# Optimization experiments

Hardware: AMD Instinct MI355X
Metric: run time of the kernel (lower is better)

Reference implementation:

```python
import jax, jax.numpy as jnp
import numpy as np

LN_EPS = 1e-5

def _ln(x, g, b):
    m = x.mean(-1, keepdims=True)
    v = ((x - m) ** 2).mean(-1, keepdims=True)
    return (x - m) * jax.lax.rsqrt(v + LN_EPS) * g + b

def setup_inputs() -> dict:
    key = jax.random.key(0)
    B, Q, K, H, NH, L = 4, 32, 8192, 1024, 16, 128
    ks = jax.random.split(key, 10)
    def p(k, shape):
        return jax.random.normal(k, shape, jnp.float32) * 0.02
    return {
        "question_emb": jax.random.normal(ks[0], (B, Q, H), jnp.float32),
        "context_emb": jax.random.normal(ks[1], (B, K, H), jnp.float32),
        "Wq_l": p(ks[2], (H, H)), "bq_l": jnp.zeros((H,), jnp.float32),
        "Wk_l": p(ks[3], (H, H)), "bk_l": jnp.zeros((H,), jnp.float32),
        "Wq_g": p(ks[4], (H, H)), "bq_g": jnp.zeros((H,), jnp.float32),
        "Wk_g": p(ks[5], (H, H)), "bk_g": jnp.zeros((H,), jnp.float32),
        "ln_g": jnp.ones((H,), jnp.float32), "ln_b": jnp.zeros((H,), jnp.float32),
        "gp_W1": p(ks[6], (2 * H, H)), "gp_b1": jnp.zeros((H,), jnp.float32),
        "gp_W2": p(ks[7], (H, 1)), "gp_b2": jnp.zeros((1,), jnp.float32),
        "num_heads": NH,
        "chunk_len": L,
    }

def reference(question_emb, context_emb, Wq_l, bq_l, Wk_l, bk_l,
              Wq_g, bq_g, Wk_g, bk_g, ln_g, ln_b,
              gp_W1, gp_b1, gp_W2, gp_b2, num_heads, chunk_len):
    B, Qn, H = question_emb.shape
    K = context_emb.shape[1]
    nh, L = num_heads, chunk_len
    d = H // nh
    J = K // L
    scale = 1.0 / np.sqrt(d)

    # ---- Global scorer: one cross-attn over all K, then per-chunk mean pooling ----
    qh = (question_emb @ Wq_g + bq_g).reshape(B, Qn, nh, d).transpose(0, 2, 1, 3)   # [B,nh,Q,d]
    kh = (context_emb @ Wk_g + bk_g).reshape(B, K, nh, d).transpose(0, 2, 1, 3)     # [B,nh,K,d]
    wg = jax.nn.softmax(jnp.einsum('bhqd,bhkd->bhqk', qh, kh) * scale, axis=-1)     # [B,nh,Q,K]
    attn = wg.mean(axis=(1, 2))                                                     # [B,K]
    global_scores = jax.nn.softmax(attn.reshape(B, J, L).mean(-1), axis=-1)         # [B,J]

    # ---- Local scorer: per-chunk cross-attn (batched over chunks), max-over-keys pooling ----
    qh_l = (question_emb @ Wq_l + bq_l).reshape(B, Qn, nh, d).transpose(0, 2, 1, 3)  # [B,nh,Q,d]
    kh_l = (context_emb @ Wk_l + bk_l).reshape(B, J, L, nh, d).transpose(0, 1, 3, 2, 4)  # [B,J,nh,L,d]
    s_l = jnp.einsum('bhqd,bjhld->bjhql', qh_l, kh_l) * scale                        # [B,J,nh,Q,L]
    w_l = jax.nn.softmax(s_l, axis=-1)
    local_scores = jax.nn.softmax(w_l.max(-1).mean(axis=(2, 3)), axis=-1)            # [B,J]

    # ---- Router: LN'd mean-pool vecs -> gate MLP -> fuse -> softmax ----
    q_vec = _ln(question_emb.mean(1), ln_g, ln_b)                                    # [B,H]
    c_vec = _ln(context_emb.reshape(B, J, L, H).mean(2), ln_g, ln_b)                 # [B,J,H]
    g_in = jnp.concatenate([jnp.broadcast_to(q_vec[:, None, :], (B, J, H)), c_vec], -1)
    h1 = jax.nn.gelu(g_in @ gp_W1 + gp_b1, approximate=False)
    gate = jax.nn.sigmoid(h1 @ gp_W2 + gp_b2)[..., 0]                                # [B,J]
    fused = gate * local_scores + (1.0 - gate) * global_scores
    final_scores = jax.nn.softmax(fused, axis=-1)                                    # [B,J]
    global_gate = final_scores.mean(-1).reshape(B, 1, 1)
    return final_scores, local_scores, global_scores, global_gate
```

## Files before the change

kernel.cpp:

```cpp
#include <hip/hip_runtime.h>
#include <math.h>

#define B_    4
#define QN    32
#define KN    8192
#define HDIM  1024
#define NHD   16
#define DH    64
#define LCH   128
#define JCH   64

typedef float f32x4 __attribute__((ext_vector_type(4)));
typedef short s16x8 __attribute__((ext_vector_type(8)));
typedef unsigned short u16;

__device__ __forceinline__ u16 f2bf(float f) {
  unsigned u = __float_as_uint(f);
  u += 0x7fffu + ((u >> 16) & 1u);
  return (u16)(u >> 16);
}

__device__ __forceinline__ float bf2f(u16 v) {
  return __uint_as_float(((unsigned)v) << 16);
}

__device__ __forceinline__ void llds16(const void* g, void* l) {
  __builtin_amdgcn_global_load_lds((const __attribute__((address_space(1))) unsigned int*)g,
                                   (__attribute__((address_space(3))) unsigned int*)l,
                                   16, 0, 0);
}

__global__ __launch_bounds__(256) void k_zero(float* __restrict__ qh, float* __restrict__ h1,
                                              float* __restrict__ qpart) {
  int i = blockIdx.x * 256 + threadIdx.x;
  float4 z = make_float4(0.f, 0.f, 0.f, 0.f);
  if (i < 65536)        ((float4*)qh)[i] = z;
  else if (i < 131072)  ((float4*)h1)[i - 65536] = z;
  else if (i < 132096)  ((float4*)qpart)[i - 131072] = z;
}

__global__ __launch_bounds__(256) void k_ctxcv(const float* __restrict__ ctx, u16* __restrict__ ctxb,
                                               const float* __restrict__ g, const float* __restrict__ lb,
                                               float* __restrict__ cvec) {
  int bj = blockIdx.x, t = threadIdx.x;
  const float* p = ctx + (size_t)bj * LCH * HDIM + t * 4;
  u16* op = ctxb + (size_t)bj * LCH * HDIM + t * 4;
  float a0 = 0, a1 = 0, a2 = 0, a3 = 0;
  for (int r = 0; r < LCH; ++r) {
    float4 v = *(const float4*)(p + (size_t)r * HDIM);
    ushort4 o;
    o.x = f2bf(v.x); o.y = f2bf(v.y); o.z = f2bf(v.z); o.w = f2bf(v.w);
    *(ushort4*)(op + (size_t)r * HDIM) = o;
    a0 += v.x; a1 += v.y; a2 += v.z; a3 += v.w;
  }
  const float sc = 1.0f / LCH;
  a0 *= sc; a1 *= sc; a2 *= sc; a3 *= sc;
  float s = a0 + a1 + a2 + a3;
  float ss = a0 * a0 + a1 * a1 + a2 * a2 + a3 * a3;
#pragma unroll
  for (int o = 1; o < 64; o <<= 1) { s += __shfl_xor(s, o, 64); ss += __shfl_xor(ss, o, 64); }
  __shared__ float sm[4], sq[4];
  int wid = t >> 6, lane = t & 63;
  if (lane == 0) { sm[wid] = s; sq[wid] = ss; }
  __syncthreads();
  float S = sm[0] + sm[1] + sm[2] + sm[3], SS = sq[0] + sq[1] + sq[2] + sq[3];
  float mu = S / HDIM;
  float inv = rsqrtf(SS / HDIM - mu * mu + 1e-5f);
  int c = t * 4;
  float4 o;
  o.x = (a0 - mu) * inv * g[c + 0] + lb[c + 0];
  o.y = (a1 - mu) * inv * g[c + 1] + lb[c + 1];
  o.z = (a2 - mu) * inv * g[c + 2] + lb[c + 2];
  o.w = (a3 - mu) * inv * g[c + 3] + lb[c + 3];
  *(float4*)&cvec[(size_t)bj * HDIM + c] = o;
}

__global__ __launch_bounds__(256) void k_gemm_f32(const float* __restrict__ A, int lda,
                                                  const float* __restrict__ Bm, int ldb,
                                                  float* __restrict__ C, int ldc, int kchunk) {
  __shared__ float As[64][17];
  __shared__ float Bs[16][64];
  int t = threadIdx.x;
  int m0 = blockIdx.x * 64, n0 = blockIdx.y * 64, k0 = blockIdx.z * kchunk;
  int tm = t >> 4, tn = t & 15;
  float c[4][4];
#pragma unroll
  for (int i = 0; i < 4; ++i)
#pragma unroll
    for (int j = 0; j < 4; ++j) c[i][j] = 0.f;
  int ra = t >> 2, ka = (t & 3) * 4;
  int kb = t >> 4, nb = (t & 15) * 4;
  for (int kk = 0; kk < kchunk; kk += 16) {
    float4 va = *(const float4*)(A + (size_t)(m0 + ra) * lda + k0 + kk + ka);
    float4 vb = *(const float4*)(Bm + (size_t)(k0 + kk + kb) * ldb + n0 + nb);
    As[ra][ka] = va.x; As[ra][ka + 1] = va.y; As[ra][ka + 2] = va.z; As[ra][ka + 3] = va.w;
    *(float4*)&Bs[kb][nb] = vb;
    __syncthreads();
#pragma unroll
    for (int kq = 0; kq < 16; ++kq) {
      float a0 = As[tm * 4 + 0][kq], a1 = As[tm * 4 + 1][kq];
      float a2 = As[tm * 4 + 2][kq], a3 = As[tm * 4 + 3][kq];
      float b0 = Bs[kq][tn * 4 + 0], b1 = Bs[kq][tn * 4 + 1];
      float b2 = Bs[kq][tn * 4 + 2], b3 = Bs[kq][tn * 4 + 3];
      c[0][0] += a0 * b0; c[0][1] += a0 * b1; c[0][2] += a0 * b2; c[0][3] += a0 * b3;
      c[1][0] += a1 * b0; c[1][1] += a1 * b1; c[1][2] += a1 * b2; c[1][3] += a1 * b3;
      c[2][0] += a2 * b0; c[2][1] += a2 * b1; c[2][2] += a2 * b2; c[2][3] += a2 * b3;
      c[3][0] += a3 * b0; c[3][1] += a3 * b1; c[3][2] += a3 * b2; c[3][3] += a3 * b3;
    }
    __syncthreads();
  }
#pragma unroll
  for (int i = 0; i < 4; ++i)
#pragma unroll
    for (int j = 0; j < 4; ++j)
      atomicAdd(&C[(size_t)(m0 + tm * 4 + i) * ldc + n0 + tn * 4 + j], c[i][j]);
}

__global__ __launch_bounds__(256) void k_gemm_qh(const float* __restrict__ A,
                                                 const float* __restrict__ Bg, const float* __restrict__ Bl,
                                                 float* __restrict__ C) {
  __shared__ float As[64][17];
  __shared__ float Bs[16][64];
  int t = threadIdx.x;
  int ny = blockIdx.y;
  const float* Bm = (ny < 16) ? Bg : Bl;
  float* Cp = (ny < 16) ? C : (C + 131072);
  int m0 = blockIdx.x * 64, n0 = (ny & 15) * 64, k0 = blockIdx.z * 128;
  int tm = t >> 4, tn = t & 15;
  float c[4][4];
#pragma unroll
  for (int i = 0; i < 4; ++i)
#pragma unroll
    for (int j = 0; j < 4; ++j) c[i][j] = 0.f;
  int ra = t >> 2, ka = (t & 3) * 4;
  int kb = t >> 4, nb = (t & 15) * 4;
  for (int kk = 0; kk < 128; kk += 16) {
    float4 va = *(const float4*)(A + (size_t)(m0 + ra) * HDIM + k0 + kk + ka);
    float4 vb = *(const float4*)(Bm + (size_t)(k0 + kk + kb) * HDIM + n0 + nb);
    As[ra][ka] = va.x; As[ra][ka + 1] = va.y; As[ra][ka + 2] = va.z; As[ra][ka + 3] = va.w;
    *(float4*)&Bs[kb][nb] = vb;
    __syncthreads();
#pragma unroll
    for (int kq = 0; kq < 16; ++kq) {
      float a0 = As[tm * 4 + 0][kq], a1 = As[tm * 4 + 1][kq];
      float a2 = As[tm * 4 + 2][kq], a3 = As[tm * 4 + 3][kq];
      float b0 = Bs[kq][tn * 4 + 0], b1 = Bs[kq][tn * 4 + 1];
      float b2 = Bs[kq][tn * 4 + 2], b3 = Bs[kq][tn * 4 + 3];
      c[0][0] += a0 * b0; c[0][1] += a0 * b1; c[0][2] += a0 * b2; c[0][3] += a0 * b3;
      c[1][0] += a1 * b0; c[1][1] += a1 * b1; c[1][2] += a1 * b2; c[1][3] += a1 * b3;
      c[2][0] += a2 * b0; c[2][1] += a2 * b1; c[2][2] += a2 * b2; c[2][3] += a2 * b3;
      c[3][0] += a3 * b0; c[3][1] += a3 * b1; c[3][2] += a3 * b2; c[3][3] += a3 * b3;
    }
    __syncthreads();
  }
#pragma unroll
  for (int i = 0; i < 4; ++i)
#pragma unroll
    for (int j = 0; j < 4; ++j)
      atomicAdd(&Cp[(size_t)(m0 + tm * 4 + i) * HDIM + n0 + tn * 4 + j], c[i][j]);
}

__global__ __launch_bounds__(256) void k_afold(const float* __restrict__ qh, const float* __restrict__ Wk_g,
                                               const float* __restrict__ Wk_l, const float* __restrict__ bq_g,
                                               const float* __restrict__ bq_l, u16* __restrict__ Ab) {
  int ct = blockIdx.x;
  int slot = blockIdx.y;
  int b = blockIdx.z;
  int s2 = slot >> 4, h = slot & 15;
  const float* qhp = qh + (size_t)(s2 * 4 + b) * QN * HDIM;
  const float* Wk = s2 ? Wk_l : Wk_g;
  const float* bq = s2 ? bq_l : bq_g;
  __shared__ float qs[QN][DH];
  int t = threadIdx.x;
  {
    int q = t >> 3, doff = (t & 7) * 8;
    const float4* src = (const float4*)(qhp + (size_t)q * HDIM + h * DH + doff);
    float4 b0 = *(const float4*)(bq + h * DH + doff);
    float4 b1 = *(const float4*)(bq + h * DH + doff + 4);
    float4 v0 = src[0], v1 = src[1];
    qs[q][doff + 0] = v0.x + b0.x; qs[q][doff + 1] = v0.y + b0.y;
    qs[q][doff + 2] = v0.z + b0.z; qs[q][doff + 3] = v0.w + b0.w;
    qs[q][doff + 4] = v1.x + b1.x; qs[q][doff + 5] = v1.y + b1.y;
    qs[q][doff + 6] = v1.z + b1.z; qs[q][doff + 7] = v1.w + b1.w;
  }
  __syncthreads();
  int c = ct * 256 + t;
  float w[DH];
  const float* wr = Wk + (size_t)c * HDIM + h * DH;
#pragma unroll
  for (int d = 0; d < DH; d += 4) {
    float4 v = *(const float4*)(wr + d);
    w[d] = v.x; w[d + 1] = v.y; w[d + 2] = v.z; w[d + 3] = v.w;
  }
  u16* outp = Ab + ((size_t)b * HDIM + s2 * 512 + h * QN) * HDIM + c;
  for (int q = 0; q < QN; ++q) {
    float acc = 0.f;
#pragma unroll
    for (int d = 0; d < DH; ++d) acc += qs[q][d] * w[d];
    outp[(size_t)q * HDIM] = f2bf(acc * 0.125f);
  }
}

__global__ __launch_bounds__(256) void k_sbias(const float* __restrict__ qh, const float* __restrict__ bk_g,
                                               const float* __restrict__ bk_l, const float* __restrict__ bq_g,
                                               const float* __restrict__ bq_l, float* __restrict__ sbias) {
  int i = blockIdx.x * 256 + threadIdx.x;
  int b = i >> 10, n = i & (HDIM - 1);
  int s2 = n >> 9, hq = n & 511, h = hq >> 5, q = hq & 31;
  const float* qr = qh + ((size_t)(s2 * 4 + b) * QN + q) * HDIM + h * DH;
  const float* bk = (s2 ? bk_l : bk_g) + h * DH;
  const float* bq = (s2 ? bq_l : bq_g) + h * DH;
  float acc = 0.f;
#pragma unroll
  for (int d = 0; d < DH; ++d) acc += (qr[d] + bq[d]) * bk[d];
  sbias[i] = acc * 0.125f;
}

__global__ __launch_bounds__(512, 2) void k_scores(const u16* __restrict__ ctxb, const u16* __restrict__ Ab,
                                                   const float* __restrict__ sbias,
                                                   float* __restrict__ mglob, float* __restrict__ zglob,
                                                   float* __restrict__ locinv) {
  __shared__ u16 lds[65536];
  u16* A0 = lds;           u16* B0 = lds + 16384;
  u16* A1 = lds + 32768;   u16* B1 = lds + 49152;
  int bid = blockIdx.x;
  int work = (bid & 7) * 64 + (bid >> 3);
  int b = work >> 7, rem = work & 127, rt = rem >> 2, nt = rem & 3;
  int t = threadIdx.x, wid = t >> 6, lane = t & 63;
  int wm = wid >> 2, wn = wid & 3;
  int lrow = lane & 15, lkg = lane >> 4;

  const u16* ctx0 = ctxb + ((size_t)b * KN + rt * 256) * HDIM;
  const u16* Afp  = Ab + ((size_t)b * HDIM + nt * 256) * HDIM;

  int grow = wid * 8 + (lane >> 3);
  int gslot = (lane & 7) ^ (lane >> 3);
  const u16* gA[4]; const u16* gB[4]; int dof[4];
#pragma unroll
  for (int s = 0; s < 4; ++s) {
    gA[s] = ctx0 + (size_t)(s * 64 + grow) * HDIM + gslot * 8;
    gB[s] = Afp + (size_t)(s * 64 + grow) * HDIM + gslot * 8;
    dof[s] = s * 4096 + wid * 512;
  }

  int rowA = (wm * 128 + lrow) * 64;
  int rowB = (wn * 64 + lrow) * 64;
  int p8[2];
#pragma unroll
  for (int ks = 0; ks < 2; ++ks) p8[ks] = ((ks * 4 + lkg) ^ (lane & 7)) * 8;

  f32x4 acc[8][4];
#pragma unroll
  for (int mi = 0; mi < 8; ++mi)
#pragma unroll
    for (int ni = 0; ni < 4; ++ni) acc[mi][ni] = 0.f;

#define STAGE(AT, BT, KT) { \
  _Pragma("unroll") for (int s = 0; s < 4; ++s) { \
    llds16(gA[s] + (KT) * 64, (AT) + dof[s]); \
    llds16(gB[s] + (KT) * 64, (BT) + dof[s]); } }

#define COMPUTE(AT, BT) { \
  _Pragma("unroll") for (int ks = 0; ks < 2; ++ks) { \
    const u16* pA = (AT) + rowA + p8[ks]; \
    const u16* pB = (BT) + rowB + p8[ks]; \
    s16x8 av[8], bv[4]; \
    _Pragma("unroll") for (int mi = 0; mi < 8; ++mi) av[mi] = *(const s16x8*)(pA + mi * 1024); \
    _Pragma("unroll") for (int ni = 0; ni < 4; ++ni) bv[ni] = *(const s16x8*)(pB + ni * 1024); \
    _Pragma("unroll") for (int mi = 0; mi < 8; ++mi) \
    _Pragma("unroll") for (int ni = 0; ni < 4; ++ni) \
      acc[mi][ni] = __builtin_amdgcn_mfma_f32_16x16x32_bf16(av[mi], bv[ni], acc[mi][ni], 0, 0, 0); } }

#define SYNCN(N) { asm volatile("s_waitcnt vmcnt(" #N ")" ::: "memory"); \
                   __builtin_amdgcn_s_barrier(); \
                   __builtin_amdgcn_sched_barrier(0); }

#define SUB(KT, CA, CB, SA, SB, FULL) { \
  if (FULL) { STAGE(SA, SB, (KT) + 1); } \
  if (FULL) { SYNCN(8) } else { SYNCN(0) } \
  __builtin_amdgcn_s_setprio(1); \
  COMPUTE(CA, CB); \
  __builtin_amdgcn_s_setprio(0); \
  __builtin_amdgcn_s_barrier(); }

  STAGE(A0, B0, 0);
  SUB(0,  A0, B0, A1, B1, 1)
  SUB(1,  A1, B1, A0, B0, 1)
  SUB(2,  A0, B0, A1, B1, 1)
  SUB(3,  A1, B1, A0, B0, 1)
  SUB(4,  A0, B0, A1, B1, 1)
  SUB(5,  A1, B1, A0, B0, 1)
  SUB(6,  A0, B0, A1, B1, 1)
  SUB(7,  A1, B1, A0, B0, 1)
  SUB(8,  A0, B0, A1, B1, 1)
  SUB(9,  A1, B1, A0, B0, 1)
  SUB(10, A0, B0, A1, B1, 1)
  SUB(11, A1, B1, A0, B0, 1)
  SUB(12, A0, B0, A1, B1, 1)
  SUB(13, A1, B1, A0, B0, 1)
  SUB(14, A0, B0, A1, B1, 1)
  SUB(15, A1, B1, A0, B0, 0)
#undef STAGE
#undef COMPUTE
#undef SYNCN
#undef SUB

  int jc = rt * 2 + wm;
  float sb[4];
#pragma unroll
  for (int ni = 0; ni < 4; ++ni)
    sb[ni] = sbias[b * HDIM + nt * 256 + wn * 64 + ni * 16 + lrow];
#pragma unroll
  for (int ni = 0; ni < 4; ++ni) {
    float m = -1e30f;
#pragma unroll
    for (int mi = 0; mi < 8; ++mi)
#pragma unroll
      for (int r = 0; r < 4; ++r) m = fmaxf(m, acc[mi][ni][r]);
    m += sb[ni];
    m = fmaxf(m, __shfl_xor(m, 16, 64));
    m = fmaxf(m, __shfl_xor(m, 32, 64));
    float z = 0.f;
#pragma unroll
    for (int mi = 0; mi < 8; ++mi)
#pragma unroll
      for (int r = 0; r < 4; ++r) z += __expf(acc[mi][ni][r] + sb[ni] - m);
    z += __shfl_xor(z, 16, 64);
    z += __shfl_xor(z, 32, 64);
    if (lane < 16) {
      int n = nt * 256 + wn * 64 + ni * 16 + lane;
      if (n < 512) {
        size_t o = ((size_t)b * 512 + n) * JCH + jc;
        mglob[o] = m; zglob[o] = z;
      } else {
        locinv[((size_t)b * JCH + jc) * 512 + (n - 512)] = 1.0f / z;
      }
    }
  }
}

__global__ __launch_bounds__(256) void k_qvec(const float* __restrict__ q, const float* __restrict__ g,
                                              const float* __restrict__ lb, float* __restrict__ qvec) {
  int b = blockIdx.x, t = threadIdx.x;
  const float* p = q + (size_t)b * QN * HDIM + t * 4;
  float a0 = 0, a1 = 0, a2 = 0, a3 = 0;
  for (int r = 0; r < QN; ++r) {
    float4 v = *(const float4*)(p + (size_t)r * HDIM);
    a0 += v.x; a1 += v.y; a2 += v.z; a3 += v.w;
  }
  const float sc = 1.0f / QN;
  a0 *= sc; a1 *= sc; a2 *= sc; a3 *= sc;
  float s = a0 + a1 + a2 + a3;
  float ss = a0 * a0 + a1 * a1 + a2 * a2 + a3 * a3;
#pragma unroll
  for (int o = 1; o < 64; o <<= 1) { s += __shfl_xor(s, o, 64); ss += __shfl_xor(ss, o, 64); }
  __shared__ float sm[4], sq[4];
  int wid = t >> 6, lane = t & 63;
  if (lane == 0) { sm[wid] = s; sq[wid] = ss; }
  __syncthreads();
  float S = sm[0] + sm[1] + sm[2] + sm[3], SS = sq[0] + sq[1] + sq[2] + sq[3];
  float mu = S / HDIM;
  float inv = rsqrtf(SS / HDIM - mu * mu + 1e-5f);
  int c = t * 4;
  float4 o;
  o.x = (a0 - mu) * inv * g[c + 0] + lb[c + 0];
  o.y = (a1 - mu) * inv * g[c + 1] + lb[c + 1];
  o.z = (a2 - mu) * inv * g[c + 2] + lb[c + 2];
  o.w = (a3 - mu) * inv * g[c + 3] + lb[c + 3];
  *(float4*)&qvec[(size_t)b * HDIM + c] = o;
}

__global__ __launch_bounds__(256) void k_qpart(const float* __restrict__ qvec, const float* __restrict__ W1,
                                               float* __restrict__ qpart) {
  int nt = blockIdx.x, b = blockIdx.y, ks = blockIdx.z;
  int n = nt * 256 + threadIdx.x;
  const float* qv = qvec + (size_t)b * HDIM + ks * 64;
  const float* wp = W1 + (size_t)ks * 64 * HDIM + n;
  float acc = 0.f;
#pragma unroll 8
  for (int c = 0; c < 64; ++c) acc += qv[c] * wp[(size_t)c * HDIM];
  atomicAdd(&qpart[(size_t)b * HDIM + n], acc);
}

__global__ __launch_bounds__(64) void k_hq(const float* __restrict__ mglob, const float* __restrict__ zglob,
                                           float* __restrict__ Mh, float* __restrict__ Zr) {
  int id = blockIdx.x * 64 + threadIdx.x;
  int b = id >> 9, hq = id & 511;
  const float* mg = mglob + ((size_t)b * 512 + hq) * JCH;
  const float* zg = zglob + ((size_t)b * 512 + hq) * JCH;
  float m = -1e30f;
  for (int j = 0; j < JCH; ++j) m = fmaxf(m, mg[j]);
  float z = 0.f;
  for (int j = 0; j < JCH; ++j) z += zg[j] * __expf(mg[j] - m);
  Mh[id] = m;
  Zr[id] = 1.0f / z;
}

__global__ __launch_bounds__(256) void k_chunk(const float* __restrict__ mglob, const float* __restrict__ zglob,
                                               const float* __restrict__ locinv,
                                               const float* __restrict__ Mh, const float* __restrict__ Zr,
                                               const float* __restrict__ h1, const float* __restrict__ qpart,
                                               const float* __restrict__ b1, const float* __restrict__ W2,
                                               float* __restrict__ abuf, float* __restrict__ lbuf,
                                               float* __restrict__ gbuf) {
  int bj = blockIdx.x, t = threadIdx.x;
  int b = bj >> 6, j = bj & 63;
  const float* mg = mglob + (size_t)b * 512 * JCH + j;
  const float* zg = zglob + (size_t)b * 512 * JCH + j;
  const float* lp = locinv + (size_t)bj * 512;
  const float* Mb = Mh + (size_t)b * 512;
  const float* Zb = Zr + (size_t)b * 512;
  float a = 0.f, l = 0.f, gsum = 0.f;
  for (int hq = t; hq < 512; hq += 256) {
    a += zg[(size_t)hq * JCH] * __expf(mg[(size_t)hq * JCH] - Mb[hq]) * Zb[hq];
    l += lp[hq];
  }
  const float* hp = h1 + (size_t)bj * HDIM;
  const float* qp = qpart + (size_t)b * HDIM;
  for (int n = t; n < HDIM; n += 256) {
    float x = hp[n] + qp[n] + b1[n];
    x = x * 0.5f * (1.0f + erff(x * 0.70710678118654752f));
    gsum += x * W2[n];
  }
#pragma unroll
  for (int o = 1; o < 64; o <<= 1) {
    a += __shfl_xor(a, o, 64); l += __shfl_xor(l, o, 64); gsum += __shfl_xor(gsum, o, 64);
  }
  __shared__ float ra[4], rl[4], rg[4];
  int wid = t >> 6, lane = t & 63;
  if (lane == 0) { ra[wid] = a; rl[wid] = l; rg[wid] = gsum; }
  __syncthreads();
  if (t == 0) {
    abuf[bj] = (ra[0] + ra[1] + ra[2] + ra[3]) * (1.0f / 65536.0f);
    lbuf[bj] = (rl[0] + rl[1] + rl[2] + rl[3]) * (1.0f / 512.0f);
    gbuf[bj] = rg[0] + rg[1] + rg[2] + rg[3];
  }
}

__global__ __launch_bounds__(64) void k_final(const float* __restrict__ abuf, const float* __restrict__ lbuf,
                                              const float* __restrict__ gbuf, const float* __restrict__ b2,
                                              float* __restrict__ out) {
  int b = blockIdx.x, t = threadIdx.x;
  float a = abuf[b * 64 + t];
  float l = lbuf[b * 64 + t];
  float gt = gbuf[b * 64 + t] + b2[0];
  gt = 1.0f / (1.0f + __expf(-gt));
  float am = a, lm = l;
#pragma unroll
  for (int o = 1; o < 64; o <<= 1) { am = fmaxf(am, __shfl_xor(am, o, 64)); lm = fmaxf(lm, __shfl_xor(lm, o, 64)); }
  float ae = __expf(a - am), le = __expf(l - lm);
  float as_ = ae, ls_ = le;
#pragma unroll
  for (int o = 1; o < 64; o <<= 1) { as_ += __shfl_xor(as_, o, 64); ls_ += __shfl_xor(ls_, o, 64); }
  float gs = ae / as_, ls = le / ls_;
  float fu = gt * ls + (1.0f - gt) * gs;
  float fm = fu;
#pragma unroll
  for (int o = 1; o < 64; o <<= 1) fm = fmaxf(fm, __shfl_xor(fm, o, 64));
  float fe = __expf(fu - fm);
  float fs_ = fe;
#pragma unroll
  for (int o = 1; o < 64; o <<= 1) fs_ += __shfl_xor(fs_, o, 64);
  float fv = fe / fs_;
  out[b * 64 + t] = fv;
  out[256 + b * 64 + t] = ls;
  out[512 + b * 64 + t] = gs;
  float tot = fv;
#pragma unroll
  for (int o = 1; o < 64; o <<= 1) tot += __shfl_xor(tot, o, 64);
  if (t == 0) out[768 + b] = tot * (1.0f / 64.0f);
}

extern "C" void kernel_launch(void* const* d_in, const int* in_sizes, int n_in,
                              void* d_out, int out_size, void* d_ws, size_t ws_size,
                              hipStream_t stream) {
  const float* question = (const float*)d_in[0];
  const float* context  = (const float*)d_in[1];
  const float* Wq_l = (const float*)d_in[2];
  const float* bq_l = (const float*)d_in[3];
  const float* Wk_l = (const float*)d_in[4];
  const float* bk_l = (const float*)d_in[5];
  const float* Wq_g = (const float*)d_in[6];
  const float* bq_g = (const float*)d_in[7];
  const float* Wk_g = (const float*)d_in[8];
  const float* bk_g = (const float*)d_in[9];
  const float* ln_g = (const float*)d_in[10];
  const float* ln_b = (const float*)d_in[11];
  const float* W1   = (const float*)d_in[12];
  const float* b1   = (const float*)d_in[13];
  const float* W2   = (const float*)d_in[14];
  const float* b2   = (const float*)d_in[15];

  char* ws = (char*)d_ws;
  u16*   ctxb   = (u16*)(ws + 0);
  u16*   Ab     = (u16*)(ws + 67108864);
  float* qh     = (float*)(ws + 75497472);
  float* sbias  = (float*)(ws + 76546048);
  float* mglob  = (float*)(ws + 76562432);
  float* zglob  = (float*)(ws + 77086720);
  float* locinv = (float*)(ws + 77611008);
  float* qvec   = (float*)(ws + 78135296);
  float* cvec   = (float*)(ws + 78151680);
  float* qpart  = (float*)(ws + 79200256);
  float* h1     = (float*)(ws + 79216640);
  float* Mh     = (float*)(ws + 80265216);
  float* Zr     = (float*)(ws + 80273408);
  float* abuf   = (float*)(ws + 80281600);
  float* lbuf   = (float*)(ws + 80282624);
  float* gbuf   = (float*)(ws + 80283648);

  hipLaunchKernelGGL(k_zero, dim3(516), dim3(256), 0, stream, qh, h1, qpart);
  hipLaunchKernelGGL(k_ctxcv, dim3(256), dim3(256), 0, stream, context, ctxb, ln_g, ln_b, cvec);
  hipLaunchKernelGGL(k_gemm_qh, dim3(2, 32, 8), dim3(256), 0, stream, question, Wq_g, Wq_l, qh);
  hipLaunchKernelGGL(k_afold, dim3(4, 32, 4), dim3(256), 0, stream, qh, Wk_g, Wk_l, bq_g, bq_l, Ab);
  hipLaunchKernelGGL(k_sbias, dim3(16), dim3(256), 0, stream, qh, bk_g, bk_l, bq_g, bq_l, sbias);
  hipLaunchKernelGGL(k_scores, dim3(512), dim3(512), 0, stream, ctxb, Ab, sbias, mglob, zglob, locinv);
  hipLaunchKernelGGL(k_qvec, dim3(4), dim3(256), 0, stream, question, ln_g, ln_b, qvec);
  hipLaunchKernelGGL(k_qpart, dim3(4, 4, 16), dim3(256), 0, stream, qvec, W1, qpart);
  hipLaunchKernelGGL(k_gemm_f32, dim3(4, 16, 8), dim3(256), 0, stream, cvec, HDIM, W1 + 1048576, HDIM, h1, HDIM, 128);
  hipLaunchKernelGGL(k_hq, dim3(32), dim3(64), 0, stream, mglob, zglob, Mh, Zr);
  hipLaunchKernelGGL(k_chunk, dim3(256), dim3(256), 0, stream, mglob, zglob, locinv, Mh, Zr, h1, qpart, b1, W2, abuf, lbuf, gbuf);
  hipLaunchKernelGGL(k_final, dim3(4), dim3(64), 0, stream, abuf, lbuf, gbuf, b2, (float*)d_out);
}
```

Measured before the change: 232.2 us.

## Merge preprocessing kernels into two heterogeneous phase launches and drop split-K atomics

```diff
diff --git a/kernel.cpp b/kernel.cpp
--- a/kernel.cpp
+++ b/kernel.cpp
@@ -20,79 +20,28 @@
   return (u16)(u >> 16);
 }
 
-__device__ __forceinline__ float bf2f(u16 v) {
-  return __uint_as_float(((unsigned)v) << 16);
-}
-
 __device__ __forceinline__ void llds16(const void* g, void* l) {
   __builtin_amdgcn_global_load_lds((const __attribute__((address_space(1))) unsigned int*)g,
                                    (__attribute__((address_space(3))) unsigned int*)l,
                                    16, 0, 0);
 }
 
-__global__ __launch_bounds__(256) void k_zero(float* __restrict__ qh, float* __restrict__ h1,
-                                              float* __restrict__ qpart) {
-  int i = blockIdx.x * 256 + threadIdx.x;
-  float4 z = make_float4(0.f, 0.f, 0.f, 0.f);
-  if (i < 65536)        ((float4*)qh)[i] = z;
-  else if (i < 131072)  ((float4*)h1)[i - 65536] = z;
-  else if (i < 132096)  ((float4*)qpart)[i - 131072] = z;
-}
-
-__global__ __launch_bounds__(256) void k_ctxcv(const float* __restrict__ ctx, u16* __restrict__ ctxb,
-                                               const float* __restrict__ g, const float* __restrict__ lb,
-                                               float* __restrict__ cvec) {
-  int bj = blockIdx.x, t = threadIdx.x;
-  const float* p = ctx + (size_t)bj * LCH * HDIM + t * 4;
-  u16* op = ctxb + (size_t)bj * LCH * HDIM + t * 4;
-  float a0 = 0, a1 = 0, a2 = 0, a3 = 0;
-  for (int r = 0; r < LCH; ++r) {
-    float4 v = *(const float4*)(p + (size_t)r * HDIM);
-    ushort4 o;
-    o.x = f2bf(v.x); o.y = f2bf(v.y); o.z = f2bf(v.z); o.w = f2bf(v.w);
-    *(ushort4*)(op + (size_t)r * HDIM) = o;
-    a0 += v.x; a1 += v.y; a2 += v.z; a3 += v.w;
-  }
-  const float sc = 1.0f / LCH;
-  a0 *= sc; a1 *= sc; a2 *= sc; a3 *= sc;
-  float s = a0 + a1 + a2 + a3;
-  float ss = a0 * a0 + a1 * a1 + a2 * a2 + a3 * a3;
-#pragma unroll
-  for (int o = 1; o < 64; o <<= 1) { s += __shfl_xor(s, o, 64); ss += __shfl_xor(ss, o, 64); }
-  __shared__ float sm[4], sq[4];
-  int wid = t >> 6, lane = t & 63;
-  if (lane == 0) { sm[wid] = s; sq[wid] = ss; }
-  __syncthreads();
-  float S = sm[0] + sm[1] + sm[2] + sm[3], SS = sq[0] + sq[1] + sq[2] + sq[3];
-  float mu = S / HDIM;
-  float inv = rsqrtf(SS / HDIM - mu * mu + 1e-5f);
-  int c = t * 4;
-  float4 o;
-  o.x = (a0 - mu) * inv * g[c + 0] + lb[c + 0];
-  o.y = (a1 - mu) * inv * g[c + 1] + lb[c + 1];
-  o.z = (a2 - mu) * inv * g[c + 2] + lb[c + 2];
-  o.w = (a3 - mu) * inv * g[c + 3] + lb[c + 3];
-  *(float4*)&cvec[(size_t)bj * HDIM + c] = o;
-}
-
-__global__ __launch_bounds__(256) void k_gemm_f32(const float* __restrict__ A, int lda,
-                                                  const float* __restrict__ Bm, int ldb,
-                                                  float* __restrict__ C, int ldc, int kchunk) {
-  __shared__ float As[64][17];
-  __shared__ float Bs[16][64];
+__device__ __forceinline__ void gemm64_direct(const float* __restrict__ A, const float* __restrict__ Bm,
+                                              float* __restrict__ C, int m0, int n0, char* smem) {
+  float (*As)[17] = (float(*)[17])smem;
+  float (*Bs)[64] = (float(*)[64])(smem + 4352);
   int t = threadIdx.x;
-  int m0 = blockIdx.x * 64, n0 = blockIdx.y * 64, k0 = blockIdx.z * kchunk;
   int tm = t >> 4, tn = t & 15;
-  float c[4][4];
-#pragma unroll
-  for (int i = 0; i < 4; ++i)
-#pragma unroll
-    for (int j = 0; j < 4; ++j) c[i][j] = 0.f;
   int ra = t >> 2, ka = (t & 3) * 4;
   int kb = t >> 4, nb = (t & 15) * 4;
-  for (int kk = 0; kk < kchunk; kk += 16) {
-    float4 va = *(const float4*)(A + (size_t)(m0 + ra) * lda + k0 + kk + ka);
-    float4 vb = *(const float4*)(Bm + (size_t)(k0 + kk + kb) * ldb + n0 + nb);
+  float c[4][4];
+#pragma unroll
+  for (int i = 0; i < 4; ++i)
+#pragma unroll
+    for (int j = 0; j < 4; ++j) c[i][j] = 0.f;
+  for (int kk = 0; kk < HDIM; kk += 16) {
+    float4 va = *(const float4*)(A + (size_t)(m0 + ra) * HDIM + kk + ka);
+    float4 vb = *(const float4*)(Bm + (size_t)(kk + kb) * HDIM + n0 + nb);
     As[ra][ka] = va.x; As[ra][ka + 1] = va.y; As[ra][ka + 2] = va.z; As[ra][ka + 3] = va.w;
     *(float4*)&Bs[kb][nb] = vb;
     __syncthreads();
@@ -113,107 +62,160 @@
   for (int i = 0; i < 4; ++i)
 #pragma unroll
     for (int j = 0; j < 4; ++j)
-      atomicAdd(&C[(size_t)(m0 + tm * 4 + i) * ldc + n0 + tn * 4 + j], c[i][j]);
-}
-
-__global__ __launch_bounds__(256) void k_gemm_qh(const float* __restrict__ A,
-                                                 const float* __restrict__ Bg, const float* __restrict__ Bl,
-                                                 float* __restrict__ C) {
-  __shared__ float As[64][17];
-  __shared__ float Bs[16][64];
-  int t = threadIdx.x;
-  int ny = blockIdx.y;
-  const float* Bm = (ny < 16) ? Bg : Bl;
-  float* Cp = (ny < 16) ? C : (C + 131072);
-  int m0 = blockIdx.x * 64, n0 = (ny & 15) * 64, k0 = blockIdx.z * 128;
-  int tm = t >> 4, tn = t & 15;
-  float c[4][4];
-#pragma unroll
-  for (int i = 0; i < 4; ++i)
-#pragma unroll
-    for (int j = 0; j < 4; ++j) c[i][j] = 0.f;
-  int ra = t >> 2, ka = (t & 3) * 4;
-  int kb = t >> 4, nb = (t & 15) * 4;
-  for (int kk = 0; kk < 128; kk += 16) {
-    float4 va = *(const float4*)(A + (size_t)(m0 + ra) * HDIM + k0 + kk + ka);
-    float4 vb = *(const float4*)(Bm + (size_t)(k0 + kk + kb) * HDIM + n0 + nb);
-    As[ra][ka] = va.x; As[ra][ka + 1] = va.y; As[ra][ka + 2] = va.z; As[ra][ka + 3] = va.w;
-    *(float4*)&Bs[kb][nb] = vb;
+      C[(size_t)(m0 + tm * 4 + i) * HDIM + n0 + tn * 4 + j] = c[i][j];
+}
+
+__global__ __launch_bounds__(256) void k_phaseA(const float* __restrict__ ctx, u16* __restrict__ ctxb,
+                                                const float* __restrict__ g, const float* __restrict__ lb,
+                                                float* __restrict__ cvec,
+                                                const float* __restrict__ question,
+                                                const float* __restrict__ Wq_g, const float* __restrict__ Wq_l,
+                                                float* __restrict__ qh, float* __restrict__ qvec,
+                                                float* __restrict__ qpart) {
+  __shared__ __align__(16) char smem[8448];
+  int blk = blockIdx.x, t = threadIdx.x;
+  if (blk < 256) {
+    int bj = blk;
+    const float* p = ctx + (size_t)bj * LCH * HDIM + t * 4;
+    u16* op = ctxb + (size_t)bj * LCH * HDIM + t * 4;
+    float a0 = 0, a1 = 0, a2 = 0, a3 = 0;
+    for (int r = 0; r < LCH; ++r) {
+      float4 v = *(const float4*)(p + (size_t)r * HDIM);
+      ushort4 o;
+      o.x = f2bf(v.x); o.y = f2bf(v.y); o.z = f2bf(v.z); o.w = f2bf(v.w);
+      *(ushort4*)(op + (size_t)r * HDIM) = o;
+      a0 += v.x; a1 += v.y; a2 += v.z; a3 += v.w;
+    }
+    const float sc = 1.0f / LCH;
+    a0 *= sc; a1 *= sc; a2 *= sc; a3 *= sc;
+    float s = a0 + a1 + a2 + a3;
+    float ss = a0 * a0 + a1 * a1 + a2 * a2 + a3 * a3;
+#pragma unroll
+    for (int o = 1; o < 64; o <<= 1) { s += __shfl_xor(s, o, 64); ss += __shfl_xor(ss, o, 64); }
+    float* sm = (float*)smem; float* sq = sm + 4;
+    int wid = t >> 6, lane = t & 63;
+    if (lane == 0) { sm[wid] = s; sq[wid] = ss; }
     __syncthreads();
-#pragma unroll
-    for (int kq = 0; kq < 16; ++kq) {
-      float a0 = As[tm * 4 + 0][kq], a1 = As[tm * 4 + 1][kq];
-      float a2 = As[tm * 4 + 2][kq], a3 = As[tm * 4 + 3][kq];
-      float b0 = Bs[kq][tn * 4 + 0], b1 = Bs[kq][tn * 4 + 1];
-      float b2 = Bs[kq][tn * 4 + 2], b3 = Bs[kq][tn * 4 + 3];
-      c[0][0] += a0 * b0; c[0][1] += a0 * b1; c[0][2] += a0 * b2; c[0][3] += a0 * b3;
-      c[1][0] += a1 * b0; c[1][1] += a1 * b1; c[1][2] += a1 * b2; c[1][3] += a1 * b3;
-      c[2][0] += a2 * b0; c[2][1] += a2 * b1; c[2][2] += a2 * b2; c[2][3] += a2 * b3;
-      c[3][0] += a3 * b0; c[3][1] += a3 * b1; c[3][2] += a3 * b2; c[3][3] += a3 * b3;
-    }
+    float S = sm[0] + sm[1] + sm[2] + sm[3], SS = sq[0] + sq[1] + sq[2] + sq[3];
+    float mu = S / HDIM;
+    float inv = rsqrtf(SS / HDIM - mu * mu + 1e-5f);
+    int c = t * 4;
+    float4 o;
+    o.x = (a0 - mu) * inv * g[c + 0] + lb[c + 0];
+    o.y = (a1 - mu) * inv * g[c + 1] + lb[c + 1];
+    o.z = (a2 - mu) * inv * g[c + 2] + lb[c + 2];
+    o.w = (a3 - mu) * inv * g[c + 3] + lb[c + 3];
+    *(float4*)&cvec[(size_t)bj * HDIM + c] = o;
+  } else if (blk < 320) {
+    int id = blk - 256;
+    int s2 = id >> 5, mt = (id >> 4) & 1, ntile = id & 15;
+    gemm64_direct(question, s2 ? Wq_l : Wq_g, qh + (size_t)s2 * 131072, mt * 64, ntile * 64, smem);
+  } else if (blk < 324) {
+    int b = blk - 320;
+    const float* p = question + (size_t)b * QN * HDIM + t * 4;
+    float a0 = 0, a1 = 0, a2 = 0, a3 = 0;
+    for (int r = 0; r < QN; ++r) {
+      float4 v = *(const float4*)(p + (size_t)r * HDIM);
+      a0 += v.x; a1 += v.y; a2 += v.z; a3 += v.w;
+    }
+    const float sc = 1.0f / QN;
+    a0 *= sc; a1 *= sc; a2 *= sc; a3 *= sc;
+    float s = a0 + a1 + a2 + a3;
+    float ss = a0 * a0 + a1 * a1 + a2 * a2 + a3 * a3;
+#pragma unroll
+    for (int o = 1; o < 64; o <<= 1) { s += __shfl_xor(s, o, 64); ss += __shfl_xor(ss, o, 64); }
+    float* sm = (float*)smem; float* sq = sm + 4;
+    int wid = t >> 6, lane = t & 63;
+    if (lane == 0) { sm[wid] = s; sq[wid] = ss; }
     __syncthreads();
-  }
-#pragma unroll
-  for (int i = 0; i < 4; ++i)
-#pragma unroll
-    for (int j = 0; j < 4; ++j)
-      atomicAdd(&Cp[(size_t)(m0 + tm * 4 + i) * HDIM + n0 + tn * 4 + j], c[i][j]);
-}
-
-__global__ __launch_bounds__(256) void k_afold(const float* __restrict__ qh, const float* __restrict__ Wk_g,
-                                               const float* __restrict__ Wk_l, const float* __restrict__ bq_g,
-                                               const float* __restrict__ bq_l, u16* __restrict__ Ab) {
-  int ct = blockIdx.x;
-  int slot = blockIdx.y;
-  int b = blockIdx.z;
-  int s2 = slot >> 4, h = slot & 15;
-  const float* qhp = qh + (size_t)(s2 * 4 + b) * QN * HDIM;
-  const float* Wk = s2 ? Wk_l : Wk_g;
-  const float* bq = s2 ? bq_l : bq_g;
-  __shared__ float qs[QN][DH];
-  int t = threadIdx.x;
-  {
-    int q = t >> 3, doff = (t & 7) * 8;
-    const float4* src = (const float4*)(qhp + (size_t)q * HDIM + h * DH + doff);
-    float4 b0 = *(const float4*)(bq + h * DH + doff);
-    float4 b1 = *(const float4*)(bq + h * DH + doff + 4);
-    float4 v0 = src[0], v1 = src[1];
-    qs[q][doff + 0] = v0.x + b0.x; qs[q][doff + 1] = v0.y + b0.y;
-    qs[q][doff + 2] = v0.z + b0.z; qs[q][doff + 3] = v0.w + b0.w;
-    qs[q][doff + 4] = v1.x + b1.x; qs[q][doff + 5] = v1.y + b1.y;
-    qs[q][doff + 6] = v1.z + b1.z; qs[q][doff + 7] = v1.w + b1.w;
-  }
-  __syncthreads();
-  int c = ct * 256 + t;
-  float w[DH];
-  const float* wr = Wk + (size_t)c * HDIM + h * DH;
-#pragma unroll
-  for (int d = 0; d < DH; d += 4) {
-    float4 v = *(const float4*)(wr + d);
-    w[d] = v.x; w[d + 1] = v.y; w[d + 2] = v.z; w[d + 3] = v.w;
-  }
-  u16* outp = Ab + ((size_t)b * HDIM + s2 * 512 + h * QN) * HDIM + c;
-  for (int q = 0; q < QN; ++q) {
+    float S = sm[0] + sm[1] + sm[2] + sm[3], SS = sq[0] + sq[1] + sq[2] + sq[3];
+    float mu = S / HDIM;
+    float inv = rsqrtf(SS / HDIM - mu * mu + 1e-5f);
+    int c = t * 4;
+    float4 o;
+    o.x = (a0 - mu) * inv * g[c + 0] + lb[c + 0];
+    o.y = (a1 - mu) * inv * g[c + 1] + lb[c + 1];
+    o.z = (a2 - mu) * inv * g[c + 2] + lb[c + 2];
+    o.w = (a3 - mu) * inv * g[c + 3] + lb[c + 3];
+    *(float4*)&qvec[(size_t)b * HDIM + c] = o;
+  } else {
+    float4 z = make_float4(0.f, 0.f, 0.f, 0.f);
+#pragma unroll
+    for (int i = 0; i < 4; ++i) ((float4*)qpart)[t * 4 + i] = z;
+  }
+}
+
+__global__ __launch_bounds__(256) void k_phaseB(const float* __restrict__ qh,
+                                                const float* __restrict__ Wk_g, const float* __restrict__ Wk_l,
+                                                const float* __restrict__ bq_g, const float* __restrict__ bq_l,
+                                                u16* __restrict__ Ab,
+                                                const float* __restrict__ bk_g, const float* __restrict__ bk_l,
+                                                float* __restrict__ sbias,
+                                                const float* __restrict__ qvec, const float* __restrict__ W1,
+                                                float* __restrict__ qpart,
+                                                const float* __restrict__ cvec, float* __restrict__ h1) {
+  __shared__ __align__(16) char smem[8448];
+  int blk = blockIdx.x, t = threadIdx.x;
+  if (blk < 512) {
+    int ct = blk & 3, slot = (blk >> 2) & 31, b = blk >> 7;
+    int s2 = slot >> 4, h = slot & 15;
+    const float* qhp = qh + (size_t)(s2 * 4 + b) * QN * HDIM;
+    const float* Wk = s2 ? Wk_l : Wk_g;
+    const float* bq = s2 ? bq_l : bq_g;
+    float (*qs)[DH] = (float(*)[DH])smem;
+    {
+      int q = t >> 3, doff = (t & 7) * 8;
+      const float4* src = (const float4*)(qhp + (size_t)q * HDIM + h * DH + doff);
+      float4 b0 = *(const float4*)(bq + h * DH + doff);
+      float4 b1 = *(const float4*)(bq + h * DH + doff + 4);
+      float4 v0 = src[0], v1 = src[1];
+      qs[q][doff + 0] = v0.x + b0.x; qs[q][doff + 1] = v0.y + b0.y;
+      qs[q][doff + 2] = v0.z + b0.z; qs[q][doff + 3] = v0.w + b0.w;
+      qs[q][doff + 4] = v1.x + b1.x; qs[q][doff + 5] = v1.y + b1.y;
+      qs[q][doff + 6] = v1.z + b1.z; qs[q][doff + 7] = v1.w + b1.w;
+    }
+    __syncthreads();
+    int c = ct * 256 + t;
+    float w[DH];
+    const float* wr = Wk + (size_t)c * HDIM + h * DH;
+#pragma unroll
+    for (int d = 0; d < DH; d += 4) {
+      float4 v = *(const float4*)(wr + d);
+      w[d] = v.x; w[d + 1] = v.y; w[d + 2] = v.z; w[d + 3] = v.w;
+    }
+    u16* outp = Ab + ((size_t)b * HDIM + s2 * 512 + h * QN) * HDIM + c;
+    for (int q = 0; q < QN; ++q) {
+      float acc = 0.f;
+#pragma unroll
+      for (int d = 0; d < DH; ++d) acc += qs[q][d] * w[d];
+      outp[(size_t)q * HDIM] = f2bf(acc * 0.125f);
+    }
+  } else if (blk < 528) {
+    int i = (blk - 512) * 256 + t;
+    int b = i >> 10, n = i & (HDIM - 1);
+    int s2 = n >> 9, hq = n & 511, h = hq >> 5, q = hq & 31;
+    const float* qr = qh + ((size_t)(s2 * 4 + b) * QN + q) * HDIM + h * DH;
+    const float* bk = (s2 ? bk_l : bk_g) + h * DH;
+    const float* bq = (s2 ? bq_l : bq_g) + h * DH;
     float acc = 0.f;
 #pragma unroll
-    for (int d = 0; d < DH; ++d) acc += qs[q][d] * w[d];
-    outp[(size_t)q * HDIM] = f2bf(acc * 0.125f);
-  }
-}
-
-__global__ __launch_bounds__(256) void k_sbias(const float* __restrict__ qh, const float* __restrict__ bk_g,
-                                               const float* __restrict__ bk_l, const float* __restrict__ bq_g,
-                                               const float* __restrict__ bq_l, float* __restrict__ sbias) {
-  int i = blockIdx.x * 256 + threadIdx.x;
-  int b = i >> 10, n = i & (HDIM - 1);
-  int s2 = n >> 9, hq = n & 511, h = hq >> 5, q = hq & 31;
-  const float* qr = qh + ((size_t)(s2 * 4 + b) * QN + q) * HDIM + h * DH;
-  const float* bk = (s2 ? bk_l : bk_g) + h * DH;
-  const float* bq = (s2 ? bq_l : bq_g) + h * DH;
-  float acc = 0.f;
-#pragma unroll
-  for (int d = 0; d < DH; ++d) acc += (qr[d] + bq[d]) * bk[d];
-  sbias[i] = acc * 0.125f;
+    for (int d = 0; d < DH; ++d) acc += (qr[d] + bq[d]) * bk[d];
+    sbias[i] = acc * 0.125f;
+  } else if (blk < 784) {
+    int id = blk - 528;
+    int nt = id & 3, b = (id >> 2) & 3, ks = id >> 4;
+    int n = nt * 256 + t;
+    const float* qv = qvec + (size_t)b * HDIM + ks * 64;
+    const float* wp = W1 + (size_t)ks * 64 * HDIM + n;
+    float acc = 0.f;
+#pragma unroll 8
+    for (int c = 0; c < 64; ++c) acc += qv[c] * wp[(size_t)c * HDIM];
+    atomicAdd(&qpart[(size_t)b * HDIM + n], acc);
+  } else {
+    int id = blk - 784;
+    int mt = id >> 4, ntile = id & 15;
+    gemm64_direct(cvec, W1 + 1048576, h1, mt * 64, ntile * 64, smem);
+  }
 }
 
 __global__ __launch_bounds__(512, 2) void k_scores(const u16* __restrict__ ctxb, const u16* __restrict__ Ab,
@@ -339,52 +341,9 @@
   }
 }
 
-__global__ __launch_bounds__(256) void k_qvec(const float* __restrict__ q, const float* __restrict__ g,
-                                              const float* __restrict__ lb, float* __restrict__ qvec) {
-  int b = blockIdx.x, t = threadIdx.x;
-  const float* p = q + (size_t)b * QN * HDIM + t * 4;
-  float a0 = 0, a1 = 0, a2 = 0, a3 = 0;
-  for (int r = 0; r < QN; ++r) {
-    float4 v = *(const float4*)(p + (size_t)r * HDIM);
-    a0 += v.x; a1 += v.y; a2 += v.z; a3 += v.w;
-  }
-  const float sc = 1.0f / QN;
-  a0 *= sc; a1 *= sc; a2 *= sc; a3 *= sc;
-  float s = a0 + a1 + a2 + a3;
-  float ss = a0 * a0 + a1 * a1 + a2 * a2 + a3 * a3;
-#pragma unroll
-  for (int o = 1; o < 64; o <<= 1) { s += __shfl_xor(s, o, 64); ss += __shfl_xor(ss, o, 64); }
-  __shared__ float sm[4], sq[4];
-  int wid = t >> 6, lane = t & 63;
-  if (lane == 0) { sm[wid] = s; sq[wid] = ss; }
-  __syncthreads();
-  float S = sm[0] + sm[1] + sm[2] + sm[3], SS = sq[0] + sq[1] + sq[2] + sq[3];
-  float mu = S / HDIM;
-  float inv = rsqrtf(SS / HDIM - mu * mu + 1e-5f);
-  int c = t * 4;
-  float4 o;
-  o.x = (a0 - mu) * inv * g[c + 0] + lb[c + 0];
-  o.y = (a1 - mu) * inv * g[c + 1] + lb[c + 1];
-  o.z = (a2 - mu) * inv * g[c + 2] + lb[c + 2];
-  o.w = (a3 - mu) * inv * g[c + 3] + lb[c + 3];
-  *(float4*)&qvec[(size_t)b * HDIM + c] = o;
-}
-
-__global__ __launch_bounds__(256) void k_qpart(const float* __restrict__ qvec, const float* __restrict__ W1,
-                                               float* __restrict__ qpart) {
-  int nt = blockIdx.x, b = blockIdx.y, ks = blockIdx.z;
-  int n = nt * 256 + threadIdx.x;
-  const float* qv = qvec + (size_t)b * HDIM + ks * 64;
-  const float* wp = W1 + (size_t)ks * 64 * HDIM + n;
-  float acc = 0.f;
-#pragma unroll 8
-  for (int c = 0; c < 64; ++c) acc += qv[c] * wp[(size_t)c * HDIM];
-  atomicAdd(&qpart[(size_t)b * HDIM + n], acc);
-}
-
-__global__ __launch_bounds__(64) void k_hq(const float* __restrict__ mglob, const float* __restrict__ zglob,
-                                           float* __restrict__ Mh, float* __restrict__ Zr) {
-  int id = blockIdx.x * 64 + threadIdx.x;
+__global__ __launch_bounds__(256) void k_hq(const float* __restrict__ mglob, const float* __restrict__ zglob,
+                                            float* __restrict__ Mh, float* __restrict__ Zr) {
+  int id = blockIdx.x * 256 + threadIdx.x;
   int b = id >> 9, hq = id & 511;
   const float* mg = mglob + ((size_t)b * 512 + hq) * JCH;
   const float* zg = zglob + ((size_t)b * 512 + hq) * JCH;
@@ -509,16 +468,12 @@
   float* lbuf   = (float*)(ws + 80282624);
   float* gbuf   = (float*)(ws + 80283648);
 
-  hipLaunchKernelGGL(k_zero, dim3(516), dim3(256), 0, stream, qh, h1, qpart);
-  hipLaunchKernelGGL(k_ctxcv, dim3(256), dim3(256), 0, stream, context, ctxb, ln_g, ln_b, cvec);
-  hipLaunchKernelGGL(k_gemm_qh, dim3(2, 32, 8), dim3(256), 0, stream, question, Wq_g, Wq_l, qh);
-  hipLaunchKernelGGL(k_afold, dim3(4, 32, 4), dim3(256), 0, stream, qh, Wk_g, Wk_l, bq_g, bq_l, Ab);
-  hipLaunchKernelGGL(k_sbias, dim3(16), dim3(256), 0, stream, qh, bk_g, bk_l, bq_g, bq_l, sbias);
+  hipLaunchKernelGGL(k_phaseA, dim3(325), dim3(256), 0, stream,
+                     context, ctxb, ln_g, ln_b, cvec, question, Wq_g, Wq_l, qh, qvec, qpart);
+  hipLaunchKernelGGL(k_phaseB, dim3(848), dim3(256), 0, stream,
+                     qh, Wk_g, Wk_l, bq_g, bq_l, Ab, bk_g, bk_l, sbias, qvec, W1, qpart, cvec, h1);
   hipLaunchKernelGGL(k_scores, dim3(512), dim3(512), 0, stream, ctxb, Ab, sbias, mglob, zglob, locinv);
-  hipLaunchKernelGGL(k_qvec, dim3(4), dim3(256), 0, stream, question, ln_g, ln_b, qvec);
-  hipLaunchKernelGGL(k_qpart, dim3(4, 4, 16), dim3(256), 0, stream, qvec, W1, qpart);
-  hipLaunchKernelGGL(k_gemm_f32, dim3(4, 16, 8), dim3(256), 0, stream, cvec, HDIM, W1 + 1048576, HDIM, h1, HDIM, 128);
-  hipLaunchKernelGGL(k_hq, dim3(32), dim3(64), 0, stream, mglob, zglob, Mh, Zr);
+  hipLaunchKernelGGL(k_hq, dim3(8), dim3(256), 0, stream, mglob, zglob, Mh, Zr);
   hipLaunchKernelGGL(k_chunk, dim3(256), dim3(256), 0, stream, mglob, zglob, locinv, Mh, Zr, h1, qpart, b1, W2, abuf, lbuf, gbuf);
   hipLaunchKernelGGL(k_final, dim3(4), dim3(64), 0, stream, abuf, lbuf, gbuf, b2, (float*)d_out);
 }
```

After: 230.4 us. Within noise of the previous version (-0.8%).
